# Performance work log

Measured on AMD Instinct MI355X. Metric: run time of the kernel, lower is better.

Reference implementation:

```python
import jax, jax.numpy as jnp
import numpy as np

B, S, ENC_U, DEC_U, IN_DIM = 128, 1024, 1024, 1024, 64


def setup_inputs() -> dict:
    key = jax.random.key(0)
    ks = jax.random.split(key, 16)
    g = lambda k, shape, fan_in: jax.random.normal(k, shape, jnp.float32) / np.sqrt(fan_in)
    inp = {
        'x': jax.random.normal(ks[0], (B, 1, IN_DIM), jnp.float32),
        'hidden': jax.random.normal(ks[1], (B, DEC_U), jnp.float32),
        'enc_output': jax.random.normal(ks[2], (B, S, ENC_U), jnp.float32),
        # attention params
        'W1': g(ks[3], (ENC_U, DEC_U), ENC_U), 'b1': jnp.zeros((DEC_U,), jnp.float32),
        'W2': g(ks[4], (DEC_U, DEC_U), DEC_U), 'b2': jnp.zeros((DEC_U,), jnp.float32),
        'V': g(ks[5], (DEC_U, 1), DEC_U), 'bV': jnp.zeros((1,), jnp.float32),
        # GRU params (keras gate order: z, r, h); input to GRU is [context; x] -> ENC_U+IN_DIM
        'Wk': g(ks[6], (ENC_U + IN_DIM, 3 * DEC_U), ENC_U + IN_DIM),
        'Wr': g(ks[7], (DEC_U, 3 * DEC_U), DEC_U),
        'bg': jnp.zeros((3 * DEC_U,), jnp.float32),
        # output projection
        'Wfc': g(ks[8], (DEC_U, IN_DIM), DEC_U), 'bfc': jnp.zeros((IN_DIM,), jnp.float32),
    }
    return inp


def reference(x, hidden, enc_output, W1, b1, W2, b2, V, bV, Wk, Wr, bg, Wfc, bfc):
    U = hidden.shape[-1]
    # --- Bahdanau additive attention ---
    # score: (B, S, 1)
    feat = jnp.tanh(enc_output @ W1 + b1 + (hidden @ W2 + b2)[:, None, :])
    score = feat @ V + bV
    attention_weights = jax.nn.softmax(score, axis=1)            # (B, S, 1)
    context = jnp.sum(attention_weights * enc_output, axis=1)    # (B, ENC_U)
    # --- concat context with decoder input (single step) ---
    gin = jnp.concatenate([context, x[:, 0, :]], axis=-1)        # (B, ENC_U+IN_DIM)
    # --- one GRU cell step (reset_after=False, gate order z,r,h) ---
    xg = gin @ Wk + bg                                           # (B, 3U)
    z = jax.nn.sigmoid(xg[:, :U] + hidden @ Wr[:, :U])
    r = jax.nn.sigmoid(xg[:, U:2 * U] + hidden @ Wr[:, U:2 * U])
    hh = jnp.tanh(xg[:, 2 * U:] + (r * hidden) @ Wr[:, 2 * U:])
    state = z * hidden + (1.0 - z) * hh                          # (B, U)
    # return_sequences output with T=1 reshaped to (B, U) then fc
    out = state @ Wfc + bfc                                      # (B, IN_DIM)
    return out, state, attention_weights
```

## Files before the change

### kernel.cpp

```cpp
#include <hip/hip_runtime.h>
#include <cstdint>

#define B_  128
#define S_  1024
#define U_  1024
#define IN_ 64

typedef unsigned short u16;
typedef __attribute__((ext_vector_type(8))) short short8v;
typedef __attribute__((ext_vector_type(4))) float f32x4;

__device__ __forceinline__ u16 f2bf(float f) {
  uint32_t u = __builtin_bit_cast(uint32_t, f);
  u += 0x7fffu + ((u >> 16) & 1u);
  return (u16)(u >> 16);
}
__device__ __forceinline__ float bf2f(u16 h) {
  uint32_t u = ((uint32_t)h) << 16;
  return __builtin_bit_cast(float, u);
}
__device__ __forceinline__ float fast_tanh(float x) {
  float e = __expf(2.0f * x);
  return 1.0f - 2.0f * __builtin_amdgcn_rcpf(e + 1.0f);
}

__global__ void conv_enc_k(const float* __restrict__ in, u16* __restrict__ out) {
  size_t tid = (size_t)blockIdx.x * blockDim.x + threadIdx.x;
  size_t stride = (size_t)gridDim.x * blockDim.x;
  const size_t n8 = (size_t)B_ * S_ * U_ / 8;
  for (size_t p = tid; p < n8; p += stride) {
    const float* src = in + p * 8;
    float4 a = *(const float4*)src;
    float4 b = *(const float4*)(src + 4);
    short8v h;
    h[0] = (short)f2bf(a.x); h[1] = (short)f2bf(a.y);
    h[2] = (short)f2bf(a.z); h[3] = (short)f2bf(a.w);
    h[4] = (short)f2bf(b.x); h[5] = (short)f2bf(b.y);
    h[6] = (short)f2bf(b.z); h[7] = (short)f2bf(b.w);
    *(short8v*)(out + p * 8) = h;
  }
}

__global__ void conv_w1t_k(const float* __restrict__ W1, u16* __restrict__ w1t) {
  __shared__ float tile[32][33];
  int tx = threadIdx.x & 31, tg = threadIdx.x >> 5;
  int nb = blockIdx.x << 5, kb = blockIdx.y << 5;
#pragma unroll
  for (int i = 0; i < 4; ++i)
    tile[tg + i * 8][tx] = W1[(size_t)(kb + tg + i * 8) * U_ + nb + tx];
  __syncthreads();
#pragma unroll
  for (int i = 0; i < 4; ++i)
    w1t[(size_t)(nb + tg + i * 8) * U_ + kb + tx] = f2bf(tile[tx][tg + i * 8]);
}

template<bool ABF16>
__global__ __launch_bounds__(256) void score_gemm_k(
    const void* __restrict__ encp, const u16* __restrict__ w1t,
    const float* __restrict__ hb, const float* __restrict__ b1,
    const float* __restrict__ b2, const float* __restrict__ Vv,
    float* __restrict__ score)
{
  __shared__ __align__(16) char lds[32768];
  const int tid  = threadIdx.x;
  const int lane = tid & 63;
  const int wid  = tid >> 6;
  const int wm = wid >> 1, wn = wid & 1;
  const int r16 = lane & 15, g4 = lane >> 4;

  int bid = blockIdx.x;
  int logical = (bid & 7) * 1024 + (bid >> 3);
  const int row0 = (logical >> 3) << 7;
  const int n0   = (logical & 7) << 7;

  f32x4 acc[4][4] = {};

  for (int kk = 0; kk < U_; kk += 64) {
    if (ABF16) {
      const u16* encb = (const u16*)encp;
#pragma unroll
      for (int qi = 0; qi < 8; ++qi) {
        int q = wid * 8 + qi;
        int r = (q << 3) + (lane >> 3);
        int c = lane & 7;
        if (q < 16) {
          int j = c ^ (r & 7);
          const u16* src = encb + (((size_t)(row0 + r)) << 10) + kk + (j << 3);
          __builtin_amdgcn_global_load_lds(
              (const __attribute__((address_space(1))) void*)src,
              (__attribute__((address_space(3))) void*)(lds + (q << 10)), 16, 0, 0);
        } else {
          int n = r - 128;
          int j = c ^ (n & 7);
          const u16* src = w1t + (((size_t)(n0 + n)) << 10) + kk + (j << 3);
          __builtin_amdgcn_global_load_lds(
              (const __attribute__((address_space(1))) void*)src,
              (__attribute__((address_space(3))) void*)(lds + (q << 10)), 16, 0, 0);
        }
      }
    } else {
#pragma unroll
      for (int qi = 0; qi < 4; ++qi) {
        int q = 16 + wid * 4 + qi;
        int n = ((q - 16) << 3) + (lane >> 3);
        int c = lane & 7;
        int j = c ^ (n & 7);
        const u16* src = w1t + (((size_t)(n0 + n)) << 10) + kk + (j << 3);
        __builtin_amdgcn_global_load_lds(
            (const __attribute__((address_space(1))) void*)src,
            (__attribute__((address_space(3))) void*)(lds + (q << 10)), 16, 0, 0);
      }
      const float* encf = (const float*)encp;
#pragma unroll
      for (int i = 0; i < 4; ++i) {
        int cg = tid * 4 + i;
        int r = cg >> 3, c = cg & 7;
        int j = c ^ (r & 7);
        const float* g = encf + (((size_t)(row0 + r)) << 10) + kk + (j << 3);
        float4 a = *(const float4*)g;
        float4 b = *(const float4*)(g + 4);
        short8v h;
        h[0] = (short)f2bf(a.x); h[1] = (short)f2bf(a.y);
        h[2] = (short)f2bf(a.z); h[3] = (short)f2bf(a.w);
        h[4] = (short)f2bf(b.x); h[5] = (short)f2bf(b.y);
        h[6] = (short)f2bf(b.z); h[7] = (short)f2bf(b.w);
        *(short8v*)(lds + (cg << 4)) = h;
      }
    }
    __syncthreads();

#pragma unroll
    for (int ks = 0; ks < 2; ++ks) {
      short8v af[4], bf[4];
#pragma unroll
      for (int mi = 0; mi < 4; ++mi) {
        int row = (wm << 6) + (mi << 4) + r16;
        int jx = (ks << 2) + g4;
        af[mi] = *(const short8v*)(lds + (row << 7) + ((jx ^ (row & 7)) << 4));
      }
#pragma unroll
      for (int ni = 0; ni < 4; ++ni) {
        int n = (wn << 6) + (ni << 4) + r16;
        int jx = (ks << 2) + g4;
        bf[ni] = *(const short8v*)(lds + 16384 + (n << 7) + ((jx ^ (n & 7)) << 4));
      }
#pragma unroll
      for (int mi = 0; mi < 4; ++mi)
#pragma unroll
        for (int ni = 0; ni < 4; ++ni)
          acc[mi][ni] = __builtin_amdgcn_mfma_f32_16x16x32_bf16(af[mi], bf[ni], acc[mi][ni], 0, 0, 0);
    }
    __syncthreads();
  }

  const int b = row0 >> 10;
  float vv[4], hbv[4];
#pragma unroll
  for (int ni = 0; ni < 4; ++ni) {
    int col = n0 + (wn << 6) + (ni << 4) + r16;
    vv[ni]  = Vv[col];
    hbv[ni] = hb[(b << 10) + col] + b1[col] + b2[col];
  }
  float rowsum[4][4];
#pragma unroll
  for (int mi = 0; mi < 4; ++mi)
#pragma unroll
    for (int j = 0; j < 4; ++j) rowsum[mi][j] = 0.0f;
#pragma unroll
  for (int mi = 0; mi < 4; ++mi)
#pragma unroll
    for (int ni = 0; ni < 4; ++ni)
#pragma unroll
      for (int j = 0; j < 4; ++j)
        rowsum[mi][j] += fast_tanh(acc[mi][ni][j] + hbv[ni]) * vv[ni];
#pragma unroll
  for (int mi = 0; mi < 4; ++mi)
#pragma unroll
    for (int j = 0; j < 4; ++j) {
      float rs = rowsum[mi][j];
      rs += __shfl_xor(rs, 1);
      rs += __shfl_xor(rs, 2);
      rs += __shfl_xor(rs, 4);
      rs += __shfl_xor(rs, 8);
      if (r16 == 0)
        atomicAdd(score + row0 + (wm << 6) + (mi << 4) + (g4 << 2) + j, rs);
    }
}

__global__ void softmax_k(const float* __restrict__ score, float* __restrict__ attn) {
  __shared__ float red[8];
  int b = blockIdx.x, t = threadIdx.x;
  float4 v = ((const float4*)(score + ((size_t)b << 10)))[t];
  float m = fmaxf(fmaxf(v.x, v.y), fmaxf(v.z, v.w));
  for (int o = 1; o < 64; o <<= 1) m = fmaxf(m, __shfl_xor(m, o));
  if ((t & 63) == 0) red[t >> 6] = m;
  __syncthreads();
  m = fmaxf(fmaxf(red[0], red[1]), fmaxf(red[2], red[3]));
  float e0 = expf(v.x - m), e1 = expf(v.y - m), e2 = expf(v.z - m), e3 = expf(v.w - m);
  float s = e0 + e1 + e2 + e3;
  for (int o = 1; o < 64; o <<= 1) s += __shfl_xor(s, o);
  if ((t & 63) == 0) red[4 + (t >> 6)] = s;
  __syncthreads();
  s = red[4] + red[5] + red[6] + red[7];
  float inv = 1.0f / s;
  float4 o4; o4.x = e0 * inv; o4.y = e1 * inv; o4.z = e2 * inv; o4.w = e3 * inv;
  ((float4*)(attn + ((size_t)b << 10)))[t] = o4;
}

template<bool ABF16>
__global__ void context_k(const void* __restrict__ encp, const float* __restrict__ attn,
                          float* __restrict__ gin) {
  __shared__ float aw[128];
  int b = blockIdx.x >> 3, sc = blockIdx.x & 7, t = threadIdx.x;
  if (t < 128) aw[t] = attn[((size_t)b << 10) + sc * 128 + t];
  __syncthreads();
  float a0 = 0.f, a1 = 0.f, a2 = 0.f, a3 = 0.f;
  size_t base = ((size_t)b << 20) + ((size_t)(sc * 128) << 10);
  for (int s = 0; s < 128; ++s) {
    float w = aw[s];
    if (ABF16) {
      ushort4 e = *(const ushort4*)((const u16*)encp + base + ((size_t)s << 10) + t * 4);
      a0 += w * bf2f(e.x); a1 += w * bf2f(e.y); a2 += w * bf2f(e.z); a3 += w * bf2f(e.w);
    } else {
      float4 e = *(const float4*)((const float*)encp + base + ((size_t)s << 10) + t * 4);
      a0 += w * e.x; a1 += w * e.y; a2 += w * e.z; a3 += w * e.w;
    }
  }
  float* g = gin + (size_t)b * 1088 + t * 4;
  atomicAdd(g + 0, a0); atomicAdd(g + 1, a1); atomicAdd(g + 2, a2); atomicAdd(g + 3, a3);
}

__global__ void ginx_k(const float* __restrict__ x, float* __restrict__ gin) {
  int i = blockIdx.x * 256 + threadIdx.x;
  int b = i >> 6, c = i & 63;
  gin[(size_t)b * 1088 + 1024 + c] = x[i];
}

__global__ __launch_bounds__(256) void gemm_splitk_k(
    const float* __restrict__ A, int lda,
    const float* __restrict__ W, int ldw,
    float* __restrict__ C, int ldc)
{
  __shared__ float As[64][68];
  __shared__ float Bs[64][64];
  int t = threadIdx.x;
  int m0 = blockIdx.x << 6, n0 = blockIdx.y << 6, k0 = blockIdx.z << 6;
#pragma unroll
  for (int q = 0; q < 4; ++q) {
    int cidx = q * 256 + t;
    int m = cidx >> 4, c4 = cidx & 15;
    float4 v = *(const float4*)(A + (size_t)(m0 + m) * lda + k0 + (c4 << 2));
    As[m][(c4 << 2) + 0] = v.x; As[m][(c4 << 2) + 1] = v.y;
    As[m][(c4 << 2) + 2] = v.z; As[m][(c4 << 2) + 3] = v.w;
  }
#pragma unroll
  for (int q = 0; q < 4; ++q) {
    int cidx = q * 256 + t;
    int k = cidx >> 4, nn = cidx & 15;
    *(float4*)&Bs[k][nn << 2] =
        *(const float4*)(W + (size_t)(k0 + k) * ldw + n0 + (nn << 2));
  }
  __syncthreads();
  int tx = t & 15, ty = t >> 4;
  float acc[4][4] = {};
#pragma unroll 8
  for (int k = 0; k < 64; ++k) {
    float a0 = As[(ty << 2) + 0][k], a1 = As[(ty << 2) + 1][k];
    float a2 = As[(ty << 2) + 2][k], a3 = As[(ty << 2) + 3][k];
    float4 bv = *(const float4*)&Bs[k][tx << 2];
    acc[0][0] += a0 * bv.x; acc[0][1] += a0 * bv.y; acc[0][2] += a0 * bv.z; acc[0][3] += a0 * bv.w;
    acc[1][0] += a1 * bv.x; acc[1][1] += a1 * bv.y; acc[1][2] += a1 * bv.z; acc[1][3] += a1 * bv.w;
    acc[2][0] += a2 * bv.x; acc[2][1] += a2 * bv.y; acc[2][2] += a2 * bv.z; acc[2][3] += a2 * bv.w;
    acc[3][0] += a3 * bv.x; acc[3][1] += a3 * bv.y; acc[3][2] += a3 * bv.z; acc[3][3] += a3 * bv.w;
  }
  int col = n0 + (tx << 2);
#pragma unroll
  for (int i = 0; i < 4; ++i) {
    int row = m0 + (ty << 2) + i;
#pragma unroll
    for (int j = 0; j < 4; ++j)
      atomicAdd(C + (size_t)row * ldc + col + j, acc[i][j]);
  }
}

__global__ void zr_k(const float* __restrict__ xg, const float* __restrict__ hr,
                     const float* __restrict__ hid, const float* __restrict__ bg,
                     float* __restrict__ z, float* __restrict__ rh) {
  int i = blockIdx.x * 256 + threadIdx.x;
  int b = i >> 10, n = i & 1023;
  float zv = xg[(size_t)b * 3072 + n] + bg[n] + hr[(size_t)b * 2048 + n];
  float rv = xg[(size_t)b * 3072 + 1024 + n] + bg[1024 + n] + hr[(size_t)b * 2048 + 1024 + n];
  zv = 1.0f / (1.0f + expf(-zv));
  rv = 1.0f / (1.0f + expf(-rv));
  z[i] = zv;
  rh[i] = rv * hid[i];
}

__global__ void state_ep_k(const float* __restrict__ hh, const float* __restrict__ xg,
                           const float* __restrict__ bg, const float* __restrict__ z,
                           const float* __restrict__ hid, float* __restrict__ state) {
  int i = blockIdx.x * 256 + threadIdx.x;
  int b = i >> 10, n = i & 1023;
  float val = hh[i] + xg[(size_t)b * 3072 + 2048 + n] + bg[2048 + n];
  float th = tanhf(val);
  float zv = z[i];
  state[i] = zv * hid[i] + (1.0f - zv) * th;
}

__global__ void out_ep_k(float* __restrict__ out, const float* __restrict__ bfc) {
  int i = blockIdx.x * 256 + threadIdx.x;
  out[i] += bfc[i & 63];
}

extern "C" void kernel_launch(void* const* d_in, const int* in_sizes, int n_in,
                              void* d_out, int out_size, void* d_ws, size_t ws_size,
                              hipStream_t stream) {
  const float* x    = (const float*)d_in[0];
  const float* hid  = (const float*)d_in[1];
  const float* enc  = (const float*)d_in[2];
  const float* W1   = (const float*)d_in[3];
  const float* b1   = (const float*)d_in[4];
  const float* W2   = (const float*)d_in[5];
  const float* b2   = (const float*)d_in[6];
  const float* Vv   = (const float*)d_in[7];
  const float* Wk   = (const float*)d_in[9];
  const float* Wr   = (const float*)d_in[10];
  const float* bg   = (const float*)d_in[11];
  const float* Wfc  = (const float*)d_in[12];
  const float* bfc  = (const float*)d_in[13];

  float* out       = (float*)d_out;
  float* state_out = out + 8192;
  float* attn_out  = out + 8192 + 131072;

  char* ws = (char*)d_ws;
  u16*   w1t   = (u16*)(ws + 0);
  float* hb    = (float*)(ws + 2097152);
  float* score = (float*)(ws + 2621440);
  float* gin   = (float*)(ws + 3145728);
  float* xg    = (float*)(ws + 3702784);
  float* hr    = (float*)(ws + 5275648);
  float* hh    = (float*)(ws + 6324224);
  float* z     = (float*)(ws + 6848512);
  float* rh    = (float*)(ws + 7372800);
  u16*   enc16 = (u16*)(ws + 8388608);
  const bool pathA = ws_size >= (8388608ULL + 268435456ULL);

  hipMemsetAsync(ws + 2097152, 0, 6848512 - 2097152, stream);
  hipMemsetAsync(out, 0, 32768, stream);

  conv_w1t_k<<<dim3(32, 32), 256, 0, stream>>>(W1, w1t);
  if (pathA) conv_enc_k<<<4096, 256, 0, stream>>>(enc, enc16);

  gemm_splitk_k<<<dim3(2, 16, 16), 256, 0, stream>>>(hid, 1024, W2, 1024, hb, 1024);

  if (pathA)
    score_gemm_k<true><<<8192, 256, 0, stream>>>(enc16, w1t, hb, b1, b2, Vv, score);
  else
    score_gemm_k<false><<<8192, 256, 0, stream>>>(enc, w1t, hb, b1, b2, Vv, score);

  softmax_k<<<128, 256, 0, stream>>>(score, attn_out);

  if (pathA) context_k<true><<<1024, 256, 0, stream>>>(enc16, attn_out, gin);
  else       context_k<false><<<1024, 256, 0, stream>>>(enc, attn_out, gin);
  ginx_k<<<32, 256, 0, stream>>>(x, gin);

  gemm_splitk_k<<<dim3(2, 48, 17), 256, 0, stream>>>(gin, 1088, Wk, 3072, xg, 3072);
  gemm_splitk_k<<<dim3(2, 32, 16), 256, 0, stream>>>(hid, 1024, Wr, 3072, hr, 2048);
  zr_k<<<512, 256, 0, stream>>>(xg, hr, hid, bg, z, rh);
  gemm_splitk_k<<<dim3(2, 16, 16), 256, 0, stream>>>(rh, 1024, Wr + 2048, 3072, hh, 1024);
  state_ep_k<<<512, 256, 0, stream>>>(hh, xg, bg, z, hid, state_out);
  gemm_splitk_k<<<dim3(2, 1, 16), 256, 0, stream>>>(state_out, 1024, Wfc, 64, out, 64);
  out_ep_k<<<32, 256, 0, stream>>>(out, bfc);
}
```

Baseline: 942.6 us.

## Replace bf16 score GEMM with 256x256-tile, 4-stage async-LDS pipelined kernel

Adds a new score GEMM for the bf16 encoder path. It uses 256x256 output tiles, 512 threads and a K-step of 32, with a 4-deep ring of LDS buffers filled by global_load_lds. Explicit vmcnt waits and barriers overlap the next tiles' loads with MFMA compute, and MFMA sections are raised in priority with s_setprio. The larger tile raises operand reuse per byte loaded, but it uses 128KB of LDS per block and a large accumulator array, which limits occupancy. The fp32 fallback path is split into its own non-templated kernel and is otherwise unchanged.

```diff
diff --git a/kernel.cpp b/kernel.cpp
--- a/kernel.cpp
+++ b/kernel.cpp
@@ -54,9 +54,120 @@
     w1t[(size_t)(nb + tg + i * 8) * U_ + kb + tx] = f2bf(tile[tx][tg + i * 8]);
 }
 
-template<bool ABF16>
-__global__ __launch_bounds__(256) void score_gemm_k(
-    const void* __restrict__ encp, const u16* __restrict__ w1t,
+__global__ __launch_bounds__(512, 2) void score_gemm2_k(
+    const u16* __restrict__ encb, const u16* __restrict__ w1t,
+    const float* __restrict__ hb, const float* __restrict__ b1,
+    const float* __restrict__ b2, const float* __restrict__ Vv,
+    float* __restrict__ score)
+{
+  __shared__ __align__(16) char lds[131072];
+  const int tid  = threadIdx.x;
+  const int lane = tid & 63;
+  const int wid  = tid >> 6;
+  const int wm = wid >> 2, wn = wid & 3;
+  const int r16 = lane & 15, g4 = lane >> 4;
+
+  int bid = blockIdx.x;
+  int logical = (bid & 7) * 256 + (bid >> 3);
+  const int row0 = (logical >> 2) << 8;
+  const int n0   = (logical & 3) << 8;
+
+  const int cx   = (g4 ^ ((r16 >> 1) & 3)) << 4;
+  const int aoff = wm * 8192 + r16 * 64 + cx;
+  const int boff = 16384 + wn * 4096 + r16 * 64 + cx;
+  const int qA   = wid << 1;
+
+  f32x4 acc[8][4] = {};
+
+  auto stage = [&](int tk) {
+    const int base = (tk & 3) << 15;
+    const int kk = tk << 5;
+#pragma unroll
+    for (int i = 0; i < 2; ++i) {
+      int q = qA + i;
+      int cg = (q << 6) + lane;
+      int row = cg >> 2, c = cg & 3;
+      int j = c ^ ((row >> 1) & 3);
+      const u16* srcA = encb + (((size_t)(row0 + row)) << 10) + kk + (j << 3);
+      __builtin_amdgcn_global_load_lds(
+          (const __attribute__((address_space(1))) void*)srcA,
+          (__attribute__((address_space(3))) void*)(lds + base + (q << 10)), 16, 0, 0);
+      const u16* srcB = w1t + (((size_t)(n0 + row)) << 10) + kk + (j << 3);
+      __builtin_amdgcn_global_load_lds(
+          (const __attribute__((address_space(1))) void*)srcB,
+          (__attribute__((address_space(3))) void*)(lds + base + 16384 + (q << 10)), 16, 0, 0);
+    }
+  };
+
+  auto compute = [&](int tk) {
+    const char* base = lds + ((tk & 3) << 15);
+    short8v af[8], bf[4];
+#pragma unroll
+    for (int mi = 0; mi < 8; ++mi)
+      af[mi] = *(const short8v*)(base + aoff + mi * 1024);
+#pragma unroll
+    for (int ni = 0; ni < 4; ++ni)
+      bf[ni] = *(const short8v*)(base + boff + ni * 1024);
+    __builtin_amdgcn_s_setprio(1);
+#pragma unroll
+    for (int mi = 0; mi < 8; ++mi)
+#pragma unroll
+      for (int ni = 0; ni < 4; ++ni)
+        acc[mi][ni] = __builtin_amdgcn_mfma_f32_16x16x32_bf16(af[mi], bf[ni], acc[mi][ni], 0, 0, 0);
+    __builtin_amdgcn_s_setprio(0);
+  };
+
+  stage(0); stage(1); stage(2);
+  for (int t = 0; t < 30; ++t) {
+    asm volatile("s_waitcnt vmcnt(8)" ::: "memory");
+    __builtin_amdgcn_s_barrier();
+    __builtin_amdgcn_sched_barrier(0);
+    if (t <= 28) stage(t + 3);
+    compute(t);
+  }
+  asm volatile("s_waitcnt vmcnt(4)" ::: "memory");
+  __builtin_amdgcn_s_barrier();
+  compute(30);
+  asm volatile("s_waitcnt vmcnt(0)" ::: "memory");
+  __builtin_amdgcn_s_barrier();
+  compute(31);
+
+  const int b = row0 >> 10;
+  float vv[4], hbv[4];
+#pragma unroll
+  for (int ni = 0; ni < 4; ++ni) {
+    int col = n0 + (wn << 6) + (ni << 4) + r16;
+    vv[ni]  = Vv[col];
+    hbv[ni] = hb[(b << 10) + col] + b1[col] + b2[col];
+  }
+  float rowsum[8][4];
+#pragma unroll
+  for (int mi = 0; mi < 8; ++mi)
+#pragma unroll
+    for (int j = 0; j < 4; ++j) rowsum[mi][j] = 0.0f;
+#pragma unroll
+  for (int mi = 0; mi < 8; ++mi)
+#pragma unroll
+    for (int ni = 0; ni < 4; ++ni)
+#pragma unroll
+      for (int j = 0; j < 4; ++j)
+        rowsum[mi][j] += fast_tanh(acc[mi][ni][j] + hbv[ni]) * vv[ni];
+#pragma unroll
+  for (int mi = 0; mi < 8; ++mi)
+#pragma unroll
+    for (int j = 0; j < 4; ++j) {
+      float rs = rowsum[mi][j];
+      rs += __shfl_xor(rs, 1);
+      rs += __shfl_xor(rs, 2);
+      rs += __shfl_xor(rs, 4);
+      rs += __shfl_xor(rs, 8);
+      if (r16 == 0)
+        atomicAdd(score + row0 + (wm << 7) + (mi << 4) + (g4 << 2) + j, rs);
+    }
+}
+
+__global__ __launch_bounds__(256) void score_gemm_f32_k(
+    const float* __restrict__ encf, const u16* __restrict__ w1t,
     const float* __restrict__ hb, const float* __restrict__ b1,
     const float* __restrict__ b2, const float* __restrict__ Vv,
     float* __restrict__ score)
@@ -67,68 +178,39 @@
   const int wid  = tid >> 6;
   const int wm = wid >> 1, wn = wid & 1;
   const int r16 = lane & 15, g4 = lane >> 4;
-
   int bid = blockIdx.x;
   int logical = (bid & 7) * 1024 + (bid >> 3);
   const int row0 = (logical >> 3) << 7;
   const int n0   = (logical & 7) << 7;
-
   f32x4 acc[4][4] = {};
-
   for (int kk = 0; kk < U_; kk += 64) {
-    if (ABF16) {
-      const u16* encb = (const u16*)encp;
-#pragma unroll
-      for (int qi = 0; qi < 8; ++qi) {
-        int q = wid * 8 + qi;
-        int r = (q << 3) + (lane >> 3);
-        int c = lane & 7;
-        if (q < 16) {
-          int j = c ^ (r & 7);
-          const u16* src = encb + (((size_t)(row0 + r)) << 10) + kk + (j << 3);
-          __builtin_amdgcn_global_load_lds(
-              (const __attribute__((address_space(1))) void*)src,
-              (__attribute__((address_space(3))) void*)(lds + (q << 10)), 16, 0, 0);
-        } else {
-          int n = r - 128;
-          int j = c ^ (n & 7);
-          const u16* src = w1t + (((size_t)(n0 + n)) << 10) + kk + (j << 3);
-          __builtin_amdgcn_global_load_lds(
-              (const __attribute__((address_space(1))) void*)src,
-              (__attribute__((address_space(3))) void*)(lds + (q << 10)), 16, 0, 0);
-        }
-      }
-    } else {
-#pragma unroll
-      for (int qi = 0; qi < 4; ++qi) {
-        int q = 16 + wid * 4 + qi;
-        int n = ((q - 16) << 3) + (lane >> 3);
-        int c = lane & 7;
-        int j = c ^ (n & 7);
-        const u16* src = w1t + (((size_t)(n0 + n)) << 10) + kk + (j << 3);
-        __builtin_amdgcn_global_load_lds(
-            (const __attribute__((address_space(1))) void*)src,
-            (__attribute__((address_space(3))) void*)(lds + (q << 10)), 16, 0, 0);
-      }
-      const float* encf = (const float*)encp;
-#pragma unroll
-      for (int i = 0; i < 4; ++i) {
-        int cg = tid * 4 + i;
-        int r = cg >> 3, c = cg & 7;
-        int j = c ^ (r & 7);
-        const float* g = encf + (((size_t)(row0 + r)) << 10) + kk + (j << 3);
-        float4 a = *(const float4*)g;
-        float4 b = *(const float4*)(g + 4);
-        short8v h;
-        h[0] = (short)f2bf(a.x); h[1] = (short)f2bf(a.y);
-        h[2] = (short)f2bf(a.z); h[3] = (short)f2bf(a.w);
-        h[4] = (short)f2bf(b.x); h[5] = (short)f2bf(b.y);
-        h[6] = (short)f2bf(b.z); h[7] = (short)f2bf(b.w);
-        *(short8v*)(lds + (cg << 4)) = h;
-      }
+#pragma unroll
+    for (int qi = 0; qi < 4; ++qi) {
+      int q = 16 + wid * 4 + qi;
+      int n = ((q - 16) << 3) + (lane >> 3);
+      int c = lane & 7;
+      int j = c ^ (n & 7);
+      const u16* src = w1t + (((size_t)(n0 + n)) << 10) + kk + (j << 3);
+      __builtin_amdgcn_global_load_lds(
+          (const __attribute__((address_space(1))) void*)src,
+          (__attribute__((address_space(3))) void*)(lds + (q << 10)), 16, 0, 0);
+    }
+#pragma unroll
+    for (int i = 0; i < 4; ++i) {
+      int cg = tid * 4 + i;
+      int r = cg >> 3, c = cg & 7;
+      int j = c ^ (r & 7);
+      const float* g = encf + (((size_t)(row0 + r)) << 10) + kk + (j << 3);
+      float4 a = *(const float4*)g;
+      float4 b = *(const float4*)(g + 4);
+      short8v h;
+      h[0] = (short)f2bf(a.x); h[1] = (short)f2bf(a.y);
+      h[2] = (short)f2bf(a.z); h[3] = (short)f2bf(a.w);
+      h[4] = (short)f2bf(b.x); h[5] = (short)f2bf(b.y);
+      h[6] = (short)f2bf(b.z); h[7] = (short)f2bf(b.w);
+      *(short8v*)(lds + (cg << 4)) = h;
     }
     __syncthreads();
-
 #pragma unroll
     for (int ks = 0; ks < 2; ++ks) {
       short8v af[4], bf[4];
@@ -152,7 +234,6 @@
     }
     __syncthreads();
   }
-
   const int b = row0 >> 10;
   float vv[4], hbv[4];
 #pragma unroll
@@ -355,9 +436,9 @@
   gemm_splitk_k<<<dim3(2, 16, 16), 256, 0, stream>>>(hid, 1024, W2, 1024, hb, 1024);
 
   if (pathA)
-    score_gemm_k<true><<<8192, 256, 0, stream>>>(enc16, w1t, hb, b1, b2, Vv, score);
+    score_gemm2_k<<<2048, 512, 0, stream>>>(enc16, w1t, hb, b1, b2, Vv, score);
   else
-    score_gemm_k<false><<<8192, 256, 0, stream>>>(enc, w1t, hb, b1, b2, Vv, score);
+    score_gemm_f32_k<<<8192, 256, 0, stream>>>(enc, w1t, hb, b1, b2, Vv, score);
 
   softmax_k<<<128, 256, 0, stream>>>(score, attn_out);
 
```

After: 817.7 us. 13.3% less time.

## Fuse fp32-to-bf16 conversion into a pipelined 256x256 score GEMM

Applied to the files above, without the earlier changes.

Drops the separate pass that converted the whole encoder output to bf16. The score GEMM now reads fp32 encoder data directly, converts it in registers and writes it into a double-buffered LDS tile, while W1 tiles stream in through global_load_lds. Tiles grow to 256x256 with 512 threads, and a hand-scheduled pipeline with explicit waitcnt, barriers and setprio overlaps loads with MFMA work. The context kernel now reads fp32 directly. This cuts the extra write and read of the bf16 copy, at the cost of one block per CU with 128KB LDS and fragile manual scheduling.

```diff
diff --git a/kernel.cpp b/kernel.cpp
--- a/kernel.cpp
+++ b/kernel.cpp
@@ -24,21 +24,13 @@
   return 1.0f - 2.0f * __builtin_amdgcn_rcpf(e + 1.0f);
 }
 
-__global__ void conv_enc_k(const float* __restrict__ in, u16* __restrict__ out) {
-  size_t tid = (size_t)blockIdx.x * blockDim.x + threadIdx.x;
-  size_t stride = (size_t)gridDim.x * blockDim.x;
-  const size_t n8 = (size_t)B_ * S_ * U_ / 8;
-  for (size_t p = tid; p < n8; p += stride) {
-    const float* src = in + p * 8;
-    float4 a = *(const float4*)src;
-    float4 b = *(const float4*)(src + 4);
-    short8v h;
-    h[0] = (short)f2bf(a.x); h[1] = (short)f2bf(a.y);
-    h[2] = (short)f2bf(a.z); h[3] = (short)f2bf(a.w);
-    h[4] = (short)f2bf(b.x); h[5] = (short)f2bf(b.y);
-    h[6] = (short)f2bf(b.z); h[7] = (short)f2bf(b.w);
-    *(short8v*)(out + p * 8) = h;
-  }
+__device__ __forceinline__ short8v pack8(float4 a, float4 b) {
+  short8v h;
+  h[0] = (short)f2bf(a.x); h[1] = (short)f2bf(a.y);
+  h[2] = (short)f2bf(a.z); h[3] = (short)f2bf(a.w);
+  h[4] = (short)f2bf(b.x); h[5] = (short)f2bf(b.y);
+  h[6] = (short)f2bf(b.z); h[7] = (short)f2bf(b.w);
+  return h;
 }
 
 __global__ void conv_w1t_k(const float* __restrict__ W1, u16* __restrict__ w1t) {
@@ -54,104 +46,157 @@
     w1t[(size_t)(nb + tg + i * 8) * U_ + kb + tx] = f2bf(tile[tx][tg + i * 8]);
 }
 
-template<bool ABF16>
-__global__ __launch_bounds__(256) void score_gemm_k(
-    const void* __restrict__ encp, const u16* __restrict__ w1t,
+__global__ __launch_bounds__(512, 1) void score_gemm4_k(
+    const float* __restrict__ encf, const u16* __restrict__ w1t,
     const float* __restrict__ hb, const float* __restrict__ b1,
     const float* __restrict__ b2, const float* __restrict__ Vv,
     float* __restrict__ score)
 {
-  __shared__ __align__(16) char lds[32768];
+  __shared__ __align__(16) char lds[131072];
   const int tid  = threadIdx.x;
   const int lane = tid & 63;
   const int wid  = tid >> 6;
-  const int wm = wid >> 1, wn = wid & 1;
+  const int wm = wid >> 2, wn = wid & 3;
   const int r16 = lane & 15, g4 = lane >> 4;
 
   int bid = blockIdx.x;
-  int logical = (bid & 7) * 1024 + (bid >> 3);
-  const int row0 = (logical >> 3) << 7;
-  const int n0   = (logical & 7) << 7;
-
-  f32x4 acc[4][4] = {};
-
-  for (int kk = 0; kk < U_; kk += 64) {
-    if (ABF16) {
-      const u16* encb = (const u16*)encp;
-#pragma unroll
-      for (int qi = 0; qi < 8; ++qi) {
-        int q = wid * 8 + qi;
-        int r = (q << 3) + (lane >> 3);
-        int c = lane & 7;
-        if (q < 16) {
-          int j = c ^ (r & 7);
-          const u16* src = encb + (((size_t)(row0 + r)) << 10) + kk + (j << 3);
-          __builtin_amdgcn_global_load_lds(
-              (const __attribute__((address_space(1))) void*)src,
-              (__attribute__((address_space(3))) void*)(lds + (q << 10)), 16, 0, 0);
-        } else {
-          int n = r - 128;
-          int j = c ^ (n & 7);
-          const u16* src = w1t + (((size_t)(n0 + n)) << 10) + kk + (j << 3);
-          __builtin_amdgcn_global_load_lds(
-              (const __attribute__((address_space(1))) void*)src,
-              (__attribute__((address_space(3))) void*)(lds + (q << 10)), 16, 0, 0);
-        }
-      }
-    } else {
-#pragma unroll
-      for (int qi = 0; qi < 4; ++qi) {
-        int q = 16 + wid * 4 + qi;
-        int n = ((q - 16) << 3) + (lane >> 3);
-        int c = lane & 7;
-        int j = c ^ (n & 7);
-        const u16* src = w1t + (((size_t)(n0 + n)) << 10) + kk + (j << 3);
-        __builtin_amdgcn_global_load_lds(
-            (const __attribute__((address_space(1))) void*)src,
-            (__attribute__((address_space(3))) void*)(lds + (q << 10)), 16, 0, 0);
-      }
-      const float* encf = (const float*)encp;
-#pragma unroll
-      for (int i = 0; i < 4; ++i) {
-        int cg = tid * 4 + i;
-        int r = cg >> 3, c = cg & 7;
-        int j = c ^ (r & 7);
-        const float* g = encf + (((size_t)(row0 + r)) << 10) + kk + (j << 3);
-        float4 a = *(const float4*)g;
-        float4 b = *(const float4*)(g + 4);
-        short8v h;
-        h[0] = (short)f2bf(a.x); h[1] = (short)f2bf(a.y);
-        h[2] = (short)f2bf(a.z); h[3] = (short)f2bf(a.w);
-        h[4] = (short)f2bf(b.x); h[5] = (short)f2bf(b.y);
-        h[6] = (short)f2bf(b.z); h[7] = (short)f2bf(b.w);
-        *(short8v*)(lds + (cg << 4)) = h;
-      }
-    }
-    __syncthreads();
-
-#pragma unroll
-    for (int ks = 0; ks < 2; ++ks) {
-      short8v af[4], bf[4];
-#pragma unroll
-      for (int mi = 0; mi < 4; ++mi) {
-        int row = (wm << 6) + (mi << 4) + r16;
-        int jx = (ks << 2) + g4;
-        af[mi] = *(const short8v*)(lds + (row << 7) + ((jx ^ (row & 7)) << 4));
-      }
-#pragma unroll
-      for (int ni = 0; ni < 4; ++ni) {
-        int n = (wn << 6) + (ni << 4) + r16;
-        int jx = (ks << 2) + g4;
-        bf[ni] = *(const short8v*)(lds + 16384 + (n << 7) + ((jx ^ (n & 7)) << 4));
-      }
-#pragma unroll
-      for (int mi = 0; mi < 4; ++mi)
-#pragma unroll
-        for (int ni = 0; ni < 4; ++ni)
-          acc[mi][ni] = __builtin_amdgcn_mfma_f32_16x16x32_bf16(af[mi], bf[ni], acc[mi][ni], 0, 0, 0);
-    }
-    __syncthreads();
-  }
+  int logical = (bid & 7) * 256 + (bid >> 3);
+  const int row0 = (logical >> 2) << 8;
+  const int n0   = (logical & 3) << 8;
+
+  const int cx   = (g4 ^ ((r16 >> 1) & 3)) << 4;
+  const int arow = (wm * 128 + r16) * 64 + cx;
+  const int brow = (wn * 64  + r16) * 64 + cx;
+
+  const int sr  = tid >> 2;
+  const int sc  = tid & 3;
+  const int sdst = sr * 64 + (((sc ^ ((sr >> 1) & 3))) << 4);
+  const float* pAf = encf + (((size_t)(row0 + sr)) << 10) + sc * 8;
+
+  const int jsw  = (tid & 3) ^ ((tid >> 3) & 3);
+  const u16* pB  = w1t + (((size_t)(n0 + sr)) << 10) + jsw * 8;
+
+  f32x4 acc[8][4] = {};
+  short8v bfr[4];
+  float4 rA0a, rA0b, rA0c, rA0d;
+  float4 rA1a, rA1b, rA1c, rA1d;
+
+#define BSTAGE(KS, KOFF) do {                                                  \
+    char* _wb = lds + _np + 32768 + (KS) * 16384 + (wid << 10);                \
+    __builtin_amdgcn_global_load_lds(                                          \
+        (const __attribute__((address_space(1))) void*)(pB + (KOFF)),          \
+        (__attribute__((address_space(3))) void*)_wb, 16, 0, 0);               \
+    __builtin_amdgcn_global_load_lds(                                          \
+        (const __attribute__((address_space(1))) void*)(pB + 131072 + (KOFF)), \
+        (__attribute__((address_space(3))) void*)(_wb + 8192), 16, 0, 0);      \
+  } while (0)
+
+#define AISSUE(Ra, Rb, Rc, Rd, KS, T1) do {                                    \
+    const float* _s = pAf + (size_t)(T1) * 64 + (KS) * 32;                     \
+    Ra = *(const float4*)_s;        Rb = *(const float4*)(_s + 4);             \
+    Rc = *(const float4*)(_s + 131072); Rd = *(const float4*)(_s + 131076);    \
+  } while (0)
+
+#define ACOMMIT(Ra, Rb, Rc, Rd, KS) do {                                       \
+    char* _d = lds + _np + (KS) * 16384 + sdst;                                \
+    *(short8v*)_d          = pack8(Ra, Rb);                                    \
+    *(short8v*)(_d + 8192) = pack8(Rc, Rd);                                    \
+  } while (0)
+
+#define RD_A(AF, M2, KS) do {                                                  \
+    const char* _ab = lds + _pb + (KS) * 16384;                                \
+    _Pragma("unroll")                                                          \
+    for (int mi = 0; mi < 4; ++mi)                                             \
+      (AF)[mi] = *(const short8v*)(_ab + arow + ((M2) * 4 + mi) * 1024);       \
+  } while (0)
+
+#define RD_B(KS) do {                                                          \
+    const char* _bb = lds + _pb + 32768 + (KS) * 16384;                        \
+    _Pragma("unroll")                                                          \
+    for (int ni = 0; ni < 4; ++ni)                                             \
+      bfr[ni] = *(const short8v*)(_bb + brow + ni * 1024);                     \
+  } while (0)
+
+#define MFMA16(M2, AF) do {                                                    \
+    __builtin_amdgcn_s_setprio(1);                                             \
+    _Pragma("unroll")                                                          \
+    for (int mi = 0; mi < 4; ++mi)                                             \
+      _Pragma("unroll")                                                        \
+      for (int ni = 0; ni < 4; ++ni)                                           \
+        acc[(M2) * 4 + mi][ni] = __builtin_amdgcn_mfma_f32_16x16x32_bf16(      \
+            (AF)[mi], bfr[ni], acc[(M2) * 4 + mi][ni], 0, 0, 0);               \
+    __builtin_amdgcn_s_setprio(0);                                             \
+  } while (0)
+
+#define LGKM0   asm volatile("s_waitcnt lgkmcnt(0)" ::: "memory")
+#define VMC(N)  asm volatile("s_waitcnt vmcnt(" #N ")" ::: "memory")
+#define SCHEDB  __builtin_amdgcn_sched_barrier(0)
+#define BARRIER __builtin_amdgcn_s_barrier()
+
+  {
+    const int _np = 0;
+    BSTAGE(0, 0); BSTAGE(1, 32);
+    AISSUE(rA0a, rA0b, rA0c, rA0d, 0, 0);
+    AISSUE(rA1a, rA1b, rA1c, rA1d, 1, 0);
+    VMC(0);
+    ACOMMIT(rA0a, rA0b, rA0c, rA0d, 0);
+    ACOMMIT(rA1a, rA1b, rA1c, rA1d, 1);
+    LGKM0;
+    BARRIER;
+  }
+
+  for (int t = 0; t < 15; ++t) {
+    const int _pb = (t & 1) << 16;
+    const int _np = _pb ^ 65536;
+    const size_t k1 = (size_t)(t + 1) << 6;
+    short8v af[4];
+    RD_A(af, 0, 0); RD_B(0);
+    BSTAGE(0, k1);
+    AISSUE(rA0a, rA0b, rA0c, rA0d, 0, t + 1);
+    BARRIER; LGKM0; SCHEDB;
+    MFMA16(0, af);
+    RD_A(af, 1, 0);
+    BSTAGE(1, k1 + 32);
+    AISSUE(rA1a, rA1b, rA1c, rA1d, 1, t + 1);
+    VMC(6);
+    ACOMMIT(rA0a, rA0b, rA0c, rA0d, 0);
+    LGKM0; BARRIER; SCHEDB;
+    MFMA16(1, af);
+    RD_A(af, 0, 1); RD_B(1);
+    VMC(0);
+    ACOMMIT(rA1a, rA1b, rA1c, rA1d, 1);
+    LGKM0; BARRIER; SCHEDB;
+    MFMA16(0, af);
+    RD_A(af, 1, 1);
+    BARRIER; LGKM0; SCHEDB;
+    MFMA16(1, af);
+  }
+  {
+    const int _pb = (15 & 1) << 16;
+    short8v af[4];
+    RD_A(af, 0, 0); RD_B(0);
+    BARRIER; LGKM0; SCHEDB;
+    MFMA16(0, af);
+    RD_A(af, 1, 0);
+    BARRIER; LGKM0; SCHEDB;
+    MFMA16(1, af);
+    RD_A(af, 0, 1); RD_B(1);
+    BARRIER; LGKM0; SCHEDB;
+    MFMA16(0, af);
+    RD_A(af, 1, 1);
+    BARRIER; LGKM0; SCHEDB;
+    MFMA16(1, af);
+  }
+#undef BSTAGE
+#undef AISSUE
+#undef ACOMMIT
+#undef RD_A
+#undef RD_B
+#undef MFMA16
+#undef LGKM0
+#undef VMC
+#undef SCHEDB
+#undef BARRIER
 
   const int b = row0 >> 10;
   float vv[4], hbv[4];
@@ -161,20 +206,20 @@
     vv[ni]  = Vv[col];
     hbv[ni] = hb[(b << 10) + col] + b1[col] + b2[col];
   }
-  float rowsum[4][4];
-#pragma unroll
-  for (int mi = 0; mi < 4; ++mi)
+  float rowsum[8][4];
+#pragma unroll
+  for (int mi = 0; mi < 8; ++mi)
 #pragma unroll
     for (int j = 0; j < 4; ++j) rowsum[mi][j] = 0.0f;
 #pragma unroll
-  for (int mi = 0; mi < 4; ++mi)
+  for (int mi = 0; mi < 8; ++mi)
 #pragma unroll
     for (int ni = 0; ni < 4; ++ni)
 #pragma unroll
       for (int j = 0; j < 4; ++j)
         rowsum[mi][j] += fast_tanh(acc[mi][ni][j] + hbv[ni]) * vv[ni];
 #pragma unroll
-  for (int mi = 0; mi < 4; ++mi)
+  for (int mi = 0; mi < 8; ++mi)
 #pragma unroll
     for (int j = 0; j < 4; ++j) {
       float rs = rowsum[mi][j];
@@ -183,7 +228,7 @@
       rs += __shfl_xor(rs, 4);
       rs += __shfl_xor(rs, 8);
       if (r16 == 0)
-        atomicAdd(score + row0 + (wm << 6) + (mi << 4) + (g4 << 2) + j, rs);
+        atomicAdd(score + row0 + (wm << 7) + (mi << 4) + (g4 << 2) + j, rs);
     }
 }
 
@@ -207,8 +252,7 @@
   ((float4*)(attn + ((size_t)b << 10)))[t] = o4;
 }
 
-template<bool ABF16>
-__global__ void context_k(const void* __restrict__ encp, const float* __restrict__ attn,
+__global__ void context_k(const float* __restrict__ encf, const float* __restrict__ attn,
                           float* __restrict__ gin) {
   __shared__ float aw[128];
   int b = blockIdx.x >> 3, sc = blockIdx.x & 7, t = threadIdx.x;
@@ -218,13 +262,8 @@
   size_t base = ((size_t)b << 20) + ((size_t)(sc * 128) << 10);
   for (int s = 0; s < 128; ++s) {
     float w = aw[s];
-    if (ABF16) {
-      ushort4 e = *(const ushort4*)((const u16*)encp + base + ((size_t)s << 10) + t * 4);
-      a0 += w * bf2f(e.x); a1 += w * bf2f(e.y); a2 += w * bf2f(e.z); a3 += w * bf2f(e.w);
-    } else {
-      float4 e = *(const float4*)((const float*)encp + base + ((size_t)s << 10) + t * 4);
-      a0 += w * e.x; a1 += w * e.y; a2 += w * e.z; a3 += w * e.w;
-    }
+    float4 e = *(const float4*)(encf + base + ((size_t)s << 10) + t * 4);
+    a0 += w * e.x; a1 += w * e.y; a2 += w * e.z; a3 += w * e.w;
   }
   float* g = gin + (size_t)b * 1088 + t * 4;
   atomicAdd(g + 0, a0); atomicAdd(g + 1, a1); atomicAdd(g + 2, a2); atomicAdd(g + 3, a3);
@@ -343,26 +382,19 @@
   float* hh    = (float*)(ws + 6324224);
   float* z     = (float*)(ws + 6848512);
   float* rh    = (float*)(ws + 7372800);
-  u16*   enc16 = (u16*)(ws + 8388608);
-  const bool pathA = ws_size >= (8388608ULL + 268435456ULL);
 
   hipMemsetAsync(ws + 2097152, 0, 6848512 - 2097152, stream);
   hipMemsetAsync(out, 0, 32768, stream);
 
   conv_w1t_k<<<dim3(32, 32), 256, 0, stream>>>(W1, w1t);
-  if (pathA) conv_enc_k<<<4096, 256, 0, stream>>>(enc, enc16);
 
   gemm_splitk_k<<<dim3(2, 16, 16), 256, 0, stream>>>(hid, 1024, W2, 1024, hb, 1024);
 
-  if (pathA)
-    score_gemm_k<true><<<8192, 256, 0, stream>>>(enc16, w1t, hb, b1, b2, Vv, score);
-  else
-    score_gemm_k<false><<<8192, 256, 0, stream>>>(enc, w1t, hb, b1, b2, Vv, score);
+  score_gemm4_k<<<2048, 512, 0, stream>>>(enc, w1t, hb, b1, b2, Vv, score);
 
   softmax_k<<<128, 256, 0, stream>>>(score, attn_out);
 
-  if (pathA) context_k<true><<<1024, 256, 0, stream>>>(enc16, attn_out, gin);
-  else       context_k<false><<<1024, 256, 0, stream>>>(enc, attn_out, gin);
+  context_k<<<1024, 256, 0, stream>>>(enc, attn_out, gin);
   ginx_k<<<32, 256, 0, stream>>>(x, gin);
 
   gemm_splitk_k<<<dim3(2, 48, 17), 256, 0, stream>>>(gin, 1088, Wk, 3072, xg, 3072);
```

Result: faster. 830.3 us (-11.9%).
